# Kernel tuning notes

Measured on AMD Instinct MI355X. Metric: run time of the kernel, lower is better.

Reference implementation:

```python
import jax, jax.numpy as jnp
import numpy as np


def setup_inputs() -> dict:
    key = jax.random.key(0)
    k1, k2, k3 = jax.random.split(key, 3)
    B, N, c = 8, 4096, 512
    heads, K, head_dim = 16, 1024, 64
    X = jax.random.normal(k1, (B, N, c), dtype=jnp.float32)
    ind = jax.random.randint(k2, (B, heads, K), 0, N, dtype=jnp.int64)
    bound = 1.0 / np.sqrt(head_dim)
    W = jax.random.uniform(k3, (heads, c, head_dim), dtype=jnp.float32,
                           minval=-bound, maxval=bound)
    return {"X": X, "ind": ind, "W": W}


def reference(X, ind, W):
    # X: (B, N, c); ind: (B, heads, K); W: (heads, c, head_dim)
    # Gather tokens per head: (B, heads, K, c)
    X_gathered = jnp.take_along_axis(
        X[:, None, :, :],                  # (B, 1, N, c)
        ind[..., None],                    # (B, heads, K, 1)
        axis=2,
    )
    # Per-head projection: (B, heads, K, head_dim)
    out = jnp.einsum('beki,eij->bekj', X_gathered, W)
    return out
```

## Files before the change

kernel.cpp:

```cpp
#include <hip/hip_runtime.h>

typedef __attribute__((ext_vector_type(8))) short short8;
typedef __attribute__((ext_vector_type(16))) float f32x16;

#define B_    8
#define N_TOK 4096
#define C_    512
#define H_    16
#define K_TOK 1024
#define D_    64
#define BM    128
#define BK    64

static __device__ inline ushort f2b(float f) {
  unsigned u = __builtin_bit_cast(unsigned, f);
  u += 0x7fff + ((u >> 16) & 1);
  return (ushort)(u >> 16);
}

__global__ __launch_bounds__(256) void wt_convert(const float* __restrict__ W,
                                                  ushort* __restrict__ WT) {
  int t = blockIdx.x * 256 + threadIdx.x;
  int h = t >> 15;
  int rem = t & 32767;
  int n = rem >> 9;
  int k = rem & 511;
  WT[t] = f2b(W[((size_t)(h << 9) + k) * D_ + n]);
}

__global__ __launch_bounds__(256) void gather_gemm(
    const float* __restrict__ X, const int* __restrict__ ind,
    const ushort* __restrict__ WT, float* __restrict__ out) {
  __shared__ ushort Asu[BM * BK];
  __shared__ ushort Bsu[D_ * BK];
  __shared__ int inds[BM];

  int bid = blockIdx.x;
  int nb = (bid & 7) * 128 + (bid >> 3);
  int b  = nb >> 7;
  int h  = (nb >> 3) & 15;
  int mt = nb & 7;

  int tid = threadIdx.x;
  if (tid < BM) inds[tid] = ind[(size_t)(b * H_ + h) * K_TOK + mt * BM + tid];
  __syncthreads();

  int lane = tid & 63;
  int wave = tid >> 6;
  int r16  = tid >> 4;
  int c4   = tid & 15;

  f32x16 acc0 = {};
  f32x16 acc1 = {};

  const float*  Xb  = X + (size_t)b * N_TOK * C_;
  const ushort* wth = WT + (size_t)(h * D_) * C_;

  int arow = (wave << 5) + (lane & 31);
  int hi   = lane >> 5;

  for (int kc = 0; kc < C_ / BK; ++kc) {
    if (kc) __syncthreads();

    float4 av[8];
#pragma unroll
    for (int rr = 0; rr < 8; ++rr) {
      int row = rr * 16 + r16;
      int idx = inds[row];
      av[rr] = *reinterpret_cast<const float4*>(
          &Xb[(size_t)idx * C_ + kc * BK + c4 * 4]);
    }
    uint4 bvv[2];
#pragma unroll
    for (int t2 = 0; t2 < 2; ++t2) {
      int lin = tid + 256 * t2;
      int n  = lin >> 3;
      int cc = lin & 7;
      bvv[t2] = *reinterpret_cast<const uint4*>(&wth[n * C_ + kc * BK + cc * 8]);
    }
#pragma unroll
    for (int rr = 0; rr < 8; ++rr) {
      int row = rr * 16 + r16;
      ushort4 w;
      w.x = f2b(av[rr].x); w.y = f2b(av[rr].y);
      w.z = f2b(av[rr].z); w.w = f2b(av[rr].w);
      int sw = (c4 >> 1) ^ (row & 7);
      *reinterpret_cast<ushort4*>(&Asu[row * 64 + sw * 8 + (c4 & 1) * 4]) = w;
    }
#pragma unroll
    for (int t2 = 0; t2 < 2; ++t2) {
      int lin = tid + 256 * t2;
      int n  = lin >> 3;
      int cc = lin & 7;
      *reinterpret_cast<uint4*>(&Bsu[n * 64 + ((cc ^ (n & 7)) << 3)]) = bvv[t2];
    }
    __syncthreads();

#pragma unroll
    for (int kk = 0; kk < 4; ++kk) {
      int ka = kk * 2 + hi;
      short8 af = *reinterpret_cast<short8*>(
          &Asu[arow * 64 + ((ka ^ (arow & 7)) << 3)]);
      int n0  = lane & 31;
      int swb = (ka ^ (n0 & 7)) << 3;
      short8 bf0 = *reinterpret_cast<short8*>(&Bsu[n0 * 64 + swb]);
      short8 bf1 = *reinterpret_cast<short8*>(&Bsu[(n0 + 32) * 64 + swb]);
      acc0 = __builtin_amdgcn_mfma_f32_32x32x16_bf16(af, bf0, acc0, 0, 0, 0);
      acc1 = __builtin_amdgcn_mfma_f32_32x32x16_bf16(af, bf1, acc1, 0, 0, 0);
    }
  }

  size_t obase = ((size_t)(b * H_ + h) * K_TOK + mt * BM + (wave << 5)) * D_;
  int col = lane & 31;
#pragma unroll
  for (int reg = 0; reg < 16; ++reg) {
    int r = (reg & 3) + 8 * (reg >> 2) + 4 * hi;
    out[obase + (size_t)r * D_ + col]      = acc0[reg];
    out[obase + (size_t)r * D_ + 32 + col] = acc1[reg];
  }
}

extern "C" void kernel_launch(void* const* d_in, const int* in_sizes, int n_in,
                              void* d_out, int out_size, void* d_ws, size_t ws_size,
                              hipStream_t stream) {
  const float* X  = (const float*)d_in[0];
  const int*  ind = (const int*)d_in[1];
  const float* W  = (const float*)d_in[2];
  float* out = (float*)d_out;
  ushort* WT = (ushort*)d_ws;

  wt_convert<<<dim3(2048), dim3(256), 0, stream>>>(W, WT);
  gather_gemm<<<dim3(1024), dim3(256), 0, stream>>>(X, ind, WT, out);
}
```

Measured before the change: 126.2 us.

## Prefetch next K-chunk into registers and tile the weight transpose through LDS

The gather-GEMM now issues the global loads for the next K chunk into registers before the MFMA loop of the current chunk, so memory latency can overlap compute. Gather offsets are precomputed once per block, and the K loop is fully unrolled. The weight transpose/convert kernel switches from strided scalar reads to coalesced float4 loads through a shared-memory tile with vectorized stores, and launches 128 blocks instead of 2048. The register double-buffering raises register pressure, and the launch bound of 4 blocks per CU may force spills.

```diff
diff --git a/kernel.cpp b/kernel.cpp
--- a/kernel.cpp
+++ b/kernel.cpp
@@ -20,15 +20,33 @@
 
 __global__ __launch_bounds__(256) void wt_convert(const float* __restrict__ W,
                                                   ushort* __restrict__ WT) {
-  int t = blockIdx.x * 256 + threadIdx.x;
-  int h = t >> 15;
-  int rem = t & 32767;
-  int n = rem >> 9;
-  int k = rem & 511;
-  WT[t] = f2b(W[((size_t)(h << 9) + k) * D_ + n]);
+  __shared__ float tile[64][65];
+  int h   = blockIdx.x >> 3;
+  int kc0 = (blockIdx.x & 7) << 6;
+  int t   = threadIdx.x;
+  const float* Wh = W + ((size_t)h * C_ + kc0) * D_;
+#pragma unroll
+  for (int p = 0; p < 4; ++p) {
+    int k  = p * 16 + (t >> 4);
+    int n4 = (t & 15) * 4;
+    float4 v = *reinterpret_cast<const float4*>(&Wh[k * D_ + n4]);
+    tile[k][n4 + 0] = v.x; tile[k][n4 + 1] = v.y;
+    tile[k][n4 + 2] = v.z; tile[k][n4 + 3] = v.w;
+  }
+  __syncthreads();
+  ushort* WTh = WT + (size_t)h * D_ * C_;
+#pragma unroll
+  for (int p = 0; p < 4; ++p) {
+    int n  = p * 16 + (t >> 4);
+    int k4 = (t & 15) * 4;
+    ushort4 o;
+    o.x = f2b(tile[k4 + 0][n]); o.y = f2b(tile[k4 + 1][n]);
+    o.z = f2b(tile[k4 + 2][n]); o.w = f2b(tile[k4 + 3][n]);
+    *reinterpret_cast<ushort4*>(&WTh[n * C_ + kc0 + k4]) = o;
+  }
 }
 
-__global__ __launch_bounds__(256) void gather_gemm(
+__global__ __launch_bounds__(256, 4) void gather_gemm(
     const float* __restrict__ X, const int* __restrict__ ind,
     const ushort* __restrict__ WT, float* __restrict__ out) {
   __shared__ ushort Asu[BM * BK];
@@ -59,25 +77,29 @@
   int arow = (wave << 5) + (lane & 31);
   int hi   = lane >> 5;
 
+  int aoff[8];
+#pragma unroll
+  for (int rr = 0; rr < 8; ++rr)
+    aoff[rr] = inds[rr * 16 + r16] * C_ + c4 * 4;
+  int boff[2];
+#pragma unroll
+  for (int t2 = 0; t2 < 2; ++t2) {
+    int lin = tid + 256 * t2;
+    boff[t2] = (lin >> 3) * C_ + (lin & 7) * 8;
+  }
+
+  float4 av[8]; uint4 bv[2];
+#pragma unroll
+  for (int rr = 0; rr < 8; ++rr)
+    av[rr] = *reinterpret_cast<const float4*>(&Xb[aoff[rr]]);
+#pragma unroll
+  for (int t2 = 0; t2 < 2; ++t2)
+    bv[t2] = *reinterpret_cast<const uint4*>(&wth[boff[t2]]);
+
+#pragma unroll
   for (int kc = 0; kc < C_ / BK; ++kc) {
     if (kc) __syncthreads();
 
-    float4 av[8];
-#pragma unroll
-    for (int rr = 0; rr < 8; ++rr) {
-      int row = rr * 16 + r16;
-      int idx = inds[row];
-      av[rr] = *reinterpret_cast<const float4*>(
-          &Xb[(size_t)idx * C_ + kc * BK + c4 * 4]);
-    }
-    uint4 bvv[2];
-#pragma unroll
-    for (int t2 = 0; t2 < 2; ++t2) {
-      int lin = tid + 256 * t2;
-      int n  = lin >> 3;
-      int cc = lin & 7;
-      bvv[t2] = *reinterpret_cast<const uint4*>(&wth[n * C_ + kc * BK + cc * 8]);
-    }
 #pragma unroll
     for (int rr = 0; rr < 8; ++rr) {
       int row = rr * 16 + r16;
@@ -92,7 +114,17 @@
       int lin = tid + 256 * t2;
       int n  = lin >> 3;
       int cc = lin & 7;
-      *reinterpret_cast<uint4*>(&Bsu[n * 64 + ((cc ^ (n & 7)) << 3)]) = bvv[t2];
+      *reinterpret_cast<uint4*>(&Bsu[n * 64 + ((cc ^ (n & 7)) << 3)]) = bv[t2];
+    }
+
+    float4 av2[8]; uint4 bv2[2];
+    if (kc < C_ / BK - 1) {
+#pragma unroll
+      for (int rr = 0; rr < 8; ++rr)
+        av2[rr] = *reinterpret_cast<const float4*>(&Xb[aoff[rr] + (kc + 1) * BK]);
+#pragma unroll
+      for (int t2 = 0; t2 < 2; ++t2)
+        bv2[t2] = *reinterpret_cast<const uint4*>(&wth[boff[t2] + (kc + 1) * BK]);
     }
     __syncthreads();
 
@@ -107,6 +139,12 @@
       short8 bf1 = *reinterpret_cast<short8*>(&Bsu[(n0 + 32) * 64 + swb]);
       acc0 = __builtin_amdgcn_mfma_f32_32x32x16_bf16(af, bf0, acc0, 0, 0, 0);
       acc1 = __builtin_amdgcn_mfma_f32_32x32x16_bf16(af, bf1, acc1, 0, 0, 0);
+    }
+
+    if (kc < C_ / BK - 1) {
+#pragma unroll
+      for (int rr = 0; rr < 8; ++rr) av[rr] = av2[rr];
+      bv[0] = bv2[0]; bv[1] = bv2[1];
     }
   }
 
@@ -129,6 +167,6 @@
   float* out = (float*)d_out;
   ushort* WT = (ushort*)d_ws;
 
-  wt_convert<<<dim3(2048), dim3(256), 0, stream>>>(W, WT);
+  wt_convert<<<dim3(128), dim3(256), 0, stream>>>(W, WT);
   gather_gemm<<<dim3(1024), dim3(256), 0, stream>>>(X, ind, WT, out);
 }
```

Result: slower. 174.7 us (+38.4%).
